# Optimization experiments

Measured on AMD Instinct MI355X. Metric: run time of the kernel, lower is better.

Reference implementation:

```python
import jax, jax.numpy as jnp
import numpy as np

P_MINUS_1 = 1.0      # p=2 -> (p-1)
LCP_BETA = 32.0
LOG_ALPHA = float(np.log(2.0))  # alpha=2.0
KDIG = 8
N_HEAD = 16


def _rope(x, cos, sin):
    # x: (B,T,H,D), cos/sin: (T,D//2)
    d = x.shape[-1] // 2
    x1, x2 = x[..., :d], x[..., d:]
    c = cos[None, :, None, :]
    s = sin[None, :, None, :]
    return jnp.concatenate([x1 * c - x2 * s, x1 * s + x2 * c], axis=-1)


def _rms_norm(x, eps=1e-6):
    return x * jax.lax.rsqrt(jnp.mean(jnp.square(x), axis=-1, keepdims=True) + eps)


def setup_inputs() -> dict:
    key = jax.random.key(0)
    ks = jax.random.split(key, 9)
    B, T, C, H = 2, 512, 1024, N_HEAD
    D = C // H
    std = 0.02
    x = jax.random.normal(ks[0], (B, T, C), jnp.float32)
    cos = jax.random.uniform(ks[1], (T, D // 2), jnp.float32)
    sin = jax.random.uniform(ks[2], (T, D // 2), jnp.float32)
    Wq = jax.random.normal(ks[3], (C, C), jnp.float32) * std
    Wk = jax.random.normal(ks[4], (C, C), jnp.float32) * std
    Wv = jax.random.normal(ks[5], (C, C), jnp.float32) * std
    Wo = jax.random.normal(ks[6], (C, C), jnp.float32) * std
    # to_digits_* use flax default lecun_normal: std = 1/sqrt(fan_in)
    Wdq = jax.random.normal(ks[7], (D, KDIG), jnp.float32) / np.sqrt(D)
    Wdk = jax.random.normal(ks[8], (D, KDIG), jnp.float32) / np.sqrt(D)
    return {"x": x, "cos": cos, "sin": sin, "Wq": Wq, "Wk": Wk, "Wv": Wv,
            "Wo": Wo, "Wdq": Wdq, "Wdk": Wdk}


def _soft_lcp_depth(q_digits, k_digits):
    # q_digits: (B,H,Tq,K), k_digits: (B,H,Tk,K) -> (B,H,Tq,Tk)
    diff = jnp.abs(q_digits[:, :, :, None, :] - k_digits[:, :, None, :, :])
    match_prob = jnp.exp(-LCP_BETA * jnp.square(diff))
    prefix_prob = jnp.cumprod(match_prob, axis=-1)
    return jnp.sum(prefix_prob, axis=-1)


def reference(x, cos, sin, Wq, Wk, Wv, Wo, Wdq, Wdk):
    B, T, C = x.shape
    H = N_HEAD
    D = C // H
    q = (x @ Wq).reshape(B, T, H, D)
    k = (x @ Wk).reshape(B, T, H, D)
    v = (x @ Wv).reshape(B, T, H, D)
    q = _rms_norm(_rope(q, cos, sin))
    k = _rms_norm(_rope(k, cos, sin))
    q = jnp.transpose(q, (0, 2, 1, 3))  # (B,H,T,D)
    k = jnp.transpose(k, (0, 2, 1, 3))
    v = jnp.transpose(v, (0, 2, 1, 3))
    # causal keep mask (T,T), broadcast over (B,H)
    keep = jnp.tril(jnp.ones((T, T), dtype=bool))[None, None]
    q_digits = jax.nn.sigmoid((q @ Wdq).astype(jnp.float32)) * P_MINUS_1
    k_digits = jax.nn.sigmoid((k @ Wdk).astype(jnp.float32)) * P_MINUS_1
    lcp = _soft_lcp_depth(q_digits, k_digits)  # (B,H,T,T)
    weights = jnp.exp(lcp * LOG_ALPHA)
    weights = jnp.where(keep, weights, 0.0)
    denom = jnp.maximum(jnp.sum(weights, axis=-1, keepdims=True), 1e-9)
    attn = weights / denom
    y = jnp.einsum('bhqk,bhkd->bhqd', attn.astype(v.dtype), v)
    y = jnp.transpose(y, (0, 2, 1, 3)).reshape(B, T, C)
    return y @ Wo
```

## Files before the change

### kernel.cpp

```cpp
#include <hip/hip_runtime.h>

#define T_SEQ 512
#define CDIM  1024
#define NH    16
#define DH    64
#define BB    2
#define KD    8

#define BETA_LOG2E 46.16624131f
#define LOG2E      1.4426950408889634f

typedef unsigned short u16;
typedef __attribute__((ext_vector_type(8))) short bf16x8;
typedef __attribute__((ext_vector_type(4))) float f32x4;

__device__ inline u16 f2bf(float f) {
    unsigned int u = __builtin_bit_cast(unsigned int, f);
    unsigned int r = (u + 0x7fffu + ((u >> 16) & 1u)) >> 16;
    return (u16)r;
}
__device__ inline float bf2f(u16 v) {
    unsigned int u = ((unsigned int)v) << 16;
    return __builtin_bit_cast(float, u);
}

__device__ inline void gload_lds16(const void* g, void* l) {
    __builtin_amdgcn_global_load_lds(
        (const __attribute__((address_space(1))) void*)g,
        (__attribute__((address_space(3))) void*)l, 16, 0, 0);
}

__global__ __launch_bounds__(256)
void prep_kernel(const float* __restrict__ x,
                 const float* __restrict__ W0, const float* __restrict__ W1,
                 const float* __restrict__ W2, const float* __restrict__ W3,
                 u16* __restrict__ xb,
                 u16* __restrict__ T0, u16* __restrict__ T1,
                 u16* __restrict__ T2, u16* __restrict__ T3)
{
    const int tid = threadIdx.x;
    if (blockIdx.z == 4) {
        const int row = blockIdx.y * 32 + (tid >> 3);
        const int col = blockIdx.x * 32 + (tid & 7) * 4;
        float4 v = *(const float4*)&x[(size_t)row * CDIM + col];
        ushort4 o = { f2bf(v.x), f2bf(v.y), f2bf(v.z), f2bf(v.w) };
        *(ushort4*)&xb[(size_t)row * CDIM + col] = o;
        return;
    }
    __shared__ u16 tile[32][33];
    const float* W = (blockIdx.z == 0) ? W0 : (blockIdx.z == 1) ? W1
                   : (blockIdx.z == 2) ? W2 : W3;
    u16* Tt        = (blockIdx.z == 0) ? T0 : (blockIdx.z == 1) ? T1
                   : (blockIdx.z == 2) ? T2 : T3;
    const int k0 = blockIdx.y * 32, n0 = blockIdx.x * 32;
    const int r = tid >> 3, c4 = (tid & 7) * 4;

    float4 v = *(const float4*)&W[(size_t)(k0 + r) * CDIM + n0 + c4];
    tile[r][c4 + 0] = f2bf(v.x);
    tile[r][c4 + 1] = f2bf(v.y);
    tile[r][c4 + 2] = f2bf(v.z);
    tile[r][c4 + 3] = f2bf(v.w);
    __syncthreads();
    ushort4 o;
    o.x = tile[c4 + 0][r];
    o.y = tile[c4 + 1][r];
    o.z = tile[c4 + 2][r];
    o.w = tile[c4 + 3][r];
    *(ushort4*)&Tt[(size_t)(n0 + r) * CDIM + k0 + c4] = o;
}

__global__ __launch_bounds__(256)
void gemm_qkv_fused(const u16* __restrict__ A,
                    const u16* __restrict__ Bq, const u16* __restrict__ Bk,
                    const u16* __restrict__ Bv,
                    const float* __restrict__ cosp, const float* __restrict__ sinp,
                    const float* __restrict__ Wdq, const float* __restrict__ Wdk,
                    float* __restrict__ qdig, float* __restrict__ kdig,
                    u16* __restrict__ Vt)
{
    __shared__ __align__(16) char smem[32768];
    u16* As = (u16*)smem;
    u16* Bs = As + 8192;
    float* Cf = (float*)smem;

    const int wg = (blockIdx.x & 7) * 96 + (blockIdx.x >> 3);
    const int z = wg >> 8;
    const int rem = wg & 255;
    const int h = rem & 15;
    const int m0 = (rem >> 4) * 64;
    const int n0 = h * 64;

    const u16* Bt = (z == 0) ? Bq : (z == 1) ? Bk : Bv;

    const int tid = threadIdx.x;
    const int l = tid & 63, w = tid >> 6;
    const int wr = (w >> 1) * 32, wc = (w & 1) * 32;

    f32x4 acc[2][2];
    #pragma unroll
    for (int i = 0; i < 2; ++i)
        #pragma unroll
        for (int j = 0; j < 2; ++j)
            acc[i][j] = (f32x4){0.f, 0.f, 0.f, 0.f};

    for (int k0 = 0; k0 < CDIM; k0 += 128) {
        __syncthreads();
        #pragma unroll
        for (int q = 0; q < 4; ++q) {
            const int row = w * 16 + q * 4 + (l >> 4);
            const int slot = (l & 15) ^ (row & 15);
            gload_lds16(A  + (size_t)(m0 + row) * CDIM + k0 + slot * 8,
                        &As[(w * 16 + q * 4) * 128]);
            gload_lds16(Bt + (size_t)(n0 + row) * CDIM + k0 + slot * 8,
                        &Bs[(w * 16 + q * 4) * 128]);
        }
        __syncthreads();

        #pragma unroll
        for (int kh = 0; kh < 4; ++kh) {
            bf16x8 af[2], bfr[2];
            #pragma unroll
            for (int i = 0; i < 2; ++i) {
                const int ra = wr + i * 16 + (l & 15);
                const int sa = (kh * 4 + (l >> 4)) ^ (ra & 15);
                af[i] = *(const bf16x8*)&As[ra * 128 + sa * 8];
                const int rb = wc + i * 16 + (l & 15);
                const int sb = (kh * 4 + (l >> 4)) ^ (rb & 15);
                bfr[i] = *(const bf16x8*)&Bs[rb * 128 + sb * 8];
            }
            #pragma unroll
            for (int i = 0; i < 2; ++i)
                #pragma unroll
                for (int j = 0; j < 2; ++j)
                    acc[i][j] = __builtin_amdgcn_mfma_f32_16x16x32_bf16(
                        af[i], bfr[j], acc[i][j], 0, 0, 0);
        }
    }

    __syncthreads();

    if (z == 2) {
        #pragma unroll
        for (int i = 0; i < 2; ++i)
            #pragma unroll
            for (int j = 0; j < 2; ++j) {
                const int mm = wr + i * 16 + (l >> 4) * 4;
                const int dd = wc + j * 16 + (l & 15);
                #pragma unroll
                for (int r = 0; r < 4; ++r)
                    Cf[dd * 65 + mm + r] = acc[i][j][r];
            }
        __syncthreads();
        const int b = m0 >> 9, t0 = m0 & (T_SEQ - 1);
        u16* vbase = Vt + ((size_t)(b * NH + h) * 64) * T_SEQ;
        #pragma unroll
        for (int it = 0; it < 16; ++it) {
            const int d = it * 4 + w;
            vbase[(size_t)d * T_SEQ + t0 + l] = f2bf(Cf[d * 65 + l]);
        }
        return;
    }

    #pragma unroll
    for (int i = 0; i < 2; ++i)
        #pragma unroll
        for (int j = 0; j < 2; ++j) {
            const int mm = wr + i * 16 + (l >> 4) * 4;
            const int dd = wc + j * 16 + (l & 15);
            #pragma unroll
            for (int r = 0; r < 4; ++r)
                Cf[(mm + r) * 65 + dd] = acc[i][j][r];
        }

    const float* Wd = z ? Wdk : Wdq;
    float* dig = z ? kdig : qdig;

    const int dl = l & 15, rq = l >> 4;
    float wreg[4][8];
    #pragma unroll
    for (int d4 = 0; d4 < 4; ++d4) {
        *(float4*)&wreg[d4][0] = *(const float4*)&Wd[(dl + d4 * 16) * 8];
        *(float4*)&wreg[d4][4] = *(const float4*)&Wd[(dl + d4 * 16) * 8 + 4];
    }
    __syncthreads();

    for (int g = 0; g < 4; ++g) {
        const int m = w * 16 + g * 4 + rq;
        const int mg = m0 + m;
        const int b = mg >> 9, t = mg & (T_SEQ - 1);

        const float* cr = &Cf[m * 65];
        float r0 = cr[dl], r1 = cr[dl + 16], r2 = cr[dl + 32], r3 = cr[dl + 48];
        float c0 = cosp[t * 32 + dl], c1 = cosp[t * 32 + dl + 16];
        float s0 = sinp[t * 32 + dl], s1 = sinp[t * 32 + dl + 16];
        float v0 = r0 * c0 - r2 * s0;
        float v1 = r1 * c1 - r3 * s1;
        float v2 = r0 * s0 + r2 * c0;
        float v3 = r1 * s1 + r3 * c1;

        float ss = v0 * v0 + v1 * v1 + v2 * v2 + v3 * v3;
        #pragma unroll
        for (int off = 1; off < 16; off <<= 1) ss += __shfl_xor(ss, off);
        float sc = rsqrtf(ss * (1.0f / 64.0f) + 1e-6f);
        v0 *= sc; v1 *= sc; v2 *= sc; v3 *= sc;

        float zz[8];
        #pragma unroll
        for (int j = 0; j < 8; ++j)
            zz[j] = v0 * wreg[0][j] + v1 * wreg[1][j] + v2 * wreg[2][j] + v3 * wreg[3][j];
        #pragma unroll
        for (int j = 0; j < 8; ++j) {
            #pragma unroll
            for (int off = 1; off < 16; off <<= 1) zz[j] += __shfl_xor(zz[j], off);
        }
        float zsel = zz[0];
        #pragma unroll
        for (int j = 1; j < 8; ++j) zsel = (dl == j) ? zz[j] : zsel;
        if (dl < 8)
            dig[((size_t)(b * NH + h) * T_SEQ + t) * KD + dl] =
                1.0f / (1.0f + exp2f(-LOG2E * zsel));
    }
}

__global__ __launch_bounds__(256)
void attn_partial(const float* __restrict__ qdig, const float* __restrict__ kdig,
                  const u16* __restrict__ Vt,
                  u16* __restrict__ pacc, float* __restrict__ pdeng)
{
    __shared__ u16 Vs[4096];
    __shared__ u16 Ps[4096];
    __shared__ float qds[512];

    const int tid = threadIdx.x;
    const int w = tid >> 6, l = tid & 63;

    const int wg = (blockIdx.x & 7) * 144 + (blockIdx.x >> 3);
    const int tile = wg % 36;
    const int bh = wg / 36;
    const size_t bhT = (size_t)bh * T_SEQ;

    int id = tile, c = 0;
    while (id >= c + 1) { id -= (c + 1); ++c; }
    const int kt = id;
    const int k0 = kt * 64;

    const int srow = l >> 3, sslot = (l & 7) ^ srow;
    #pragma unroll
    for (int q2 = 0; q2 < 2; ++q2) {
        const int R0 = w * 16 + q2 * 8;
        gload_lds16(Vt + ((size_t)bh * 64 + R0 + srow) * T_SEQ + k0 + sslot * 8,
                    &Vs[R0 * 64]);
    }
    *(float2*)&qds[tid * 2] = *(const float2*)&qdig[(bhT + c * 64) * KD + tid * 2];

    float kd[8];
    {
        const float* kp = &kdig[(bhT + k0 + l) * KD];
        *(float4*)&kd[0] = *(const float4*)kp;
        *(float4*)&kd[4] = *(const float4*)(kp + 4);
    }
    __syncthreads();

    const bool diag = (kt == c);
    for (int qi = 0; qi < 16; ++qi) {
        const int qrow = w * 16 + qi;
        float qd[8];
        *(float4*)&qd[0] = *(const float4*)&qds[qrow * 8];
        *(float4*)&qd[4] = *(const float4*)&qds[qrow * 8 + 4];
        float S = 0.f, lcp = 0.f;
        #pragma unroll
        for (int jj = 0; jj < 8; ++jj) {
            float d = qd[jj] - kd[jj];
            S += d * d;
            lcp += exp2f(-BETA_LOG2E * S);
        }
        float wgt = exp2f(lcp);
        if (diag && l > qrow) wgt = 0.f;
        Ps[qrow * 64 + (((l >> 3) ^ (qi & 7)) << 3) + (l & 7)] = f2bf(wgt);
    }
    __syncthreads();

    const int wr = (w >> 1) * 32, wc = (w & 1) * 32;
    f32x4 acc[2][2], accd[2];
    #pragma unroll
    for (int i = 0; i < 2; ++i) {
        accd[i] = (f32x4){0.f, 0.f, 0.f, 0.f};
        #pragma unroll
        for (int j = 0; j < 2; ++j) acc[i][j] = (f32x4){0.f, 0.f, 0.f, 0.f};
    }
    bf16x8 ones;
    #pragma unroll
    for (int i = 0; i < 8; ++i) ones[i] = (short)0x3F80;

    #pragma unroll
    for (int kh = 0; kh < 2; ++kh) {
        bf16x8 af[2], bfr[2];
        #pragma unroll
        for (int i = 0; i < 2; ++i) {
            const int ra = wr + i * 16 + (l & 15);
            const int sa = (kh * 4 + (l >> 4)) ^ (ra & 7);
            af[i] = *(const bf16x8*)&Ps[ra * 64 + sa * 8];
            const int rb = wc + i * 16 + (l & 15);
            const int sb = (kh * 4 + (l >> 4)) ^ (rb & 7);
            bfr[i] = *(const bf16x8*)&Vs[rb * 64 + sb * 8];
        }
        #pragma unroll
        for (int i = 0; i < 2; ++i) {
            accd[i] = __builtin_amdgcn_mfma_f32_16x16x32_bf16(af[i], ones, accd[i], 0, 0, 0);
            #pragma unroll
            for (int j = 0; j < 2; ++j)
                acc[i][j] = __builtin_amdgcn_mfma_f32_16x16x32_bf16(
                    af[i], bfr[j], acc[i][j], 0, 0, 0);
        }
    }

    const int task = bh * 36 + tile;
    u16* pa = pacc + (size_t)task * 4096;
    #pragma unroll
    for (int i = 0; i < 2; ++i) {
        const int row = wr + i * 16 + (l >> 4) * 4;
        #pragma unroll
        for (int j = 0; j < 2; ++j) {
            const int col = wc + j * 16 + (l & 15);
            #pragma unroll
            for (int r = 0; r < 4; ++r)
                pa[(size_t)(row + r) * 64 + col] = f2bf(acc[i][j][r]);
        }
        if ((l & 15) == 0) {
            #pragma unroll
            for (int r = 0; r < 4; ++r)
                pdeng[(size_t)task * 64 + row + r] = accd[i][r];
        }
    }
}

__global__ __launch_bounds__(256)
void attn_combine(const u16* __restrict__ pacc, const float* __restrict__ pdeng,
                  u16* __restrict__ y)
{
    const int c = blockIdx.x >> 1, half = blockIdx.x & 1;
    const int h = blockIdx.y, b = blockIdx.z;
    const int tid = threadIdx.x;
    const int r = tid >> 2, cg = (tid & 3) * 8 + half * 32;
    const int base = (b * NH + h) * 36 + c * (c + 1) / 2;

    float acc[8] = {};
    float den = 0.f;
    for (int kt = 0; kt <= c; ++kt) {
        const u16* pa = pacc + (size_t)(base + kt) * 4096 + r * 64 + cg;
        ushort4 v0 = *(const ushort4*)(pa + 0);
        ushort4 v1 = *(const ushort4*)(pa + 4);
        acc[0] += bf2f(v0.x); acc[1] += bf2f(v0.y);
        acc[2] += bf2f(v0.z); acc[3] += bf2f(v0.w);
        acc[4] += bf2f(v1.x); acc[5] += bf2f(v1.y);
        acc[6] += bf2f(v1.z); acc[7] += bf2f(v1.w);
        den += pdeng[(size_t)(base + kt) * 64 + r];
    }
    float inv = 1.f / fmaxf(den, 1e-9f);

    u16* yr = y + ((size_t)(b * T_SEQ + c * 64 + r)) * CDIM + h * DH + cg;
    uint4 p;
    p.x = f2bf(acc[0] * inv) | ((unsigned)f2bf(acc[1] * inv) << 16);
    p.y = f2bf(acc[2] * inv) | ((unsigned)f2bf(acc[3] * inv) << 16);
    p.z = f2bf(acc[4] * inv) | ((unsigned)f2bf(acc[5] * inv) << 16);
    p.w = f2bf(acc[6] * inv) | ((unsigned)f2bf(acc[7] * inv) << 16);
    *(uint4*)yr = p;
}

__global__ __launch_bounds__(256)
void gemm_proj(const u16* __restrict__ A, const u16* __restrict__ Bt,
               float* __restrict__ C)
{
    __shared__ u16 As[32 * 128];
    __shared__ u16 Bs[64 * 128];

    const int wg = (blockIdx.x & 7) * 64 + (blockIdx.x >> 3);
    const int n0 = (wg & 15) * 64;
    const int m0 = (wg >> 4) * 32;

    const int tid = threadIdx.x;
    const int l = tid & 63, w = tid >> 6;
    const int wr = (w & 1) * 16, wc = (w >> 1) * 32;

    f32x4 acc[2];
    acc[0] = (f32x4){0.f, 0.f, 0.f, 0.f};
    acc[1] = (f32x4){0.f, 0.f, 0.f, 0.f};

    for (int k0 = 0; k0 < CDIM; k0 += 128) {
        __syncthreads();
        #pragma unroll
        for (int q = 0; q < 2; ++q) {
            const int rowa = w * 8 + q * 4 + (l >> 4);
            const int slota = (l & 15) ^ (rowa & 15);
            gload_lds16(A + (size_t)(m0 + rowa) * CDIM + k0 + slota * 8,
                        &As[(w * 8 + q * 4) * 128]);
        }
        #pragma unroll
        for (int q = 0; q < 4; ++q) {
            const int row = w * 16 + q * 4 + (l >> 4);
            const int slot = (l & 15) ^ (row & 15);
            gload_lds16(Bt + (size_t)(n0 + row) * CDIM + k0 + slot * 8,
                        &Bs[(w * 16 + q * 4) * 128]);
        }
        __syncthreads();

        #pragma unroll
        for (int kh = 0; kh < 4; ++kh) {
            const int ra = wr + (l & 15);
            const int sa = (kh * 4 + (l >> 4)) ^ (ra & 15);
            bf16x8 af = *(const bf16x8*)&As[ra * 128 + sa * 8];
            #pragma unroll
            for (int j = 0; j < 2; ++j) {
                const int rb = wc + j * 16 + (l & 15);
                const int sb = (kh * 4 + (l >> 4)) ^ (rb & 15);
                bf16x8 bfr = *(const bf16x8*)&Bs[rb * 128 + sb * 8];
                acc[j] = __builtin_amdgcn_mfma_f32_16x16x32_bf16(
                    af, bfr, acc[j], 0, 0, 0);
            }
        }
    }

    #pragma unroll
    for (int j = 0; j < 2; ++j) {
        const int row = m0 + wr + (l >> 4) * 4;
        const int col = n0 + wc + j * 16 + (l & 15);
        #pragma unroll
        for (int r = 0; r < 4; ++r)
            C[(size_t)(row + r) * CDIM + col] = acc[j][r];
    }
}

extern "C" void kernel_launch(void* const* d_in, const int* in_sizes, int n_in,
                              void* d_out, int out_size, void* d_ws, size_t ws_size,
                              hipStream_t stream)
{
    (void)in_sizes; (void)n_in; (void)out_size; (void)ws_size;
    const float* x    = (const float*)d_in[0];
    const float* cosp = (const float*)d_in[1];
    const float* sinp = (const float*)d_in[2];
    const float* Wq   = (const float*)d_in[3];
    const float* Wk   = (const float*)d_in[4];
    const float* Wv   = (const float*)d_in[5];
    const float* Wo   = (const float*)d_in[6];
    const float* Wdq  = (const float*)d_in[7];
    const float* Wdk  = (const float*)d_in[8];
    float* out = (float*)d_out;

    const int M = BB * T_SEQ;
    const size_t MC = (size_t)M * CDIM;
    char* p = (char*)d_ws;
    float* qdig = (float*)p; p += (size_t)M * NH * KD * 4;
    float* kdig = (float*)p; p += (size_t)M * NH * KD * 4;
    u16* xb   = (u16*)p; p += MC * 2;
    u16* wqt  = (u16*)p; p += MC * 2;
    u16* wkt  = (u16*)p; p += MC * 2;
    u16* wvt  = (u16*)p; p += MC * 2;
    u16* wot  = (u16*)p; p += MC * 2;
    u16* Vt   = (u16*)p; p += MC * 2;
    u16* ybuf = (u16*)p; p += MC * 2;
    u16* pacc = (u16*)p; p += (size_t)1152 * 4096 * 2;
    float* pdeng = (float*)p; p += (size_t)1152 * 64 * 4;

    dim3 blk(256);
    prep_kernel<<<dim3(32, 32, 5), blk, 0, stream>>>(
        x, Wq, Wk, Wv, Wo, xb, wqt, wkt, wvt, wot);
    gemm_qkv_fused<<<dim3(768), blk, 0, stream>>>(
        xb, wqt, wkt, wvt, cosp, sinp, Wdq, Wdk, qdig, kdig, Vt);
    attn_partial<<<dim3(1152), blk, 0, stream>>>(
        qdig, kdig, Vt, pacc, pdeng);
    attn_combine<<<dim3(16, NH, BB), blk, 0, stream>>>(pacc, pdeng, ybuf);
    gemm_proj<<<dim3(512), blk, 0, stream>>>(ybuf, wot, out);
}
```

Baseline: 58.72 us.

## Double-buffer GEMM K-loops and fuse attention combine via last-block atomic counter

Both the QKV and projection GEMMs now use a double-buffered K-loop with 64-wide K tiles. Each loop prefetches the next tile with global-to-LDS loads while the current one is consumed, and uses partial vmcnt waits instead of two full syncthreads per iteration. The separate attn_combine kernel is removed. The last attn_partial block to finish for each query tile, detected through an atomic counter zeroed in prep_kernel, performs the reduction and normalization. This removes one kernel launch and overlaps load latency with MFMA work, at the cost of atomics, threadfences and a serialized tail reduction in the winning block.

New measurement: 120.2 us. +104.8%, slower.

```diff
diff --git a/kernel.cpp b/kernel.cpp
--- a/kernel.cpp
+++ b/kernel.cpp
@@ -36,10 +36,12 @@
                  const float* __restrict__ W2, const float* __restrict__ W3,
                  u16* __restrict__ xb,
                  u16* __restrict__ T0, u16* __restrict__ T1,
-                 u16* __restrict__ T2, u16* __restrict__ T3)
+                 u16* __restrict__ T2, u16* __restrict__ T3,
+                 int* __restrict__ cnt)
 {
     const int tid = threadIdx.x;
     if (blockIdx.z == 4) {
+        if (blockIdx.x == 0 && blockIdx.y == 0) cnt[tid] = 0;
         const int row = blockIdx.y * 32 + (tid >> 3);
         const int col = blockIdx.x * 32 + (tid & 7) * 4;
         float4 v = *(const float4*)&x[(size_t)row * CDIM + col];
@@ -95,6 +97,8 @@
     const int tid = threadIdx.x;
     const int l = tid & 63, w = tid >> 6;
     const int wr = (w >> 1) * 32, wc = (w & 1) * 32;
+    const int srow = l >> 3;
+    const int sslot = (l & 7) ^ srow;
 
     f32x4 acc[2][2];
     #pragma unroll
@@ -103,40 +107,53 @@
         for (int j = 0; j < 2; ++j)
             acc[i][j] = (f32x4){0.f, 0.f, 0.f, 0.f};
 
-    for (int k0 = 0; k0 < CDIM; k0 += 128) {
-        __syncthreads();
-        #pragma unroll
-        for (int q = 0; q < 4; ++q) {
-            const int row = w * 16 + q * 4 + (l >> 4);
-            const int slot = (l & 15) ^ (row & 15);
-            gload_lds16(A  + (size_t)(m0 + row) * CDIM + k0 + slot * 8,
-                        &As[(w * 16 + q * 4) * 128]);
-            gload_lds16(Bt + (size_t)(n0 + row) * CDIM + k0 + slot * 8,
-                        &Bs[(w * 16 + q * 4) * 128]);
-        }
-        __syncthreads();
-
-        #pragma unroll
-        for (int kh = 0; kh < 4; ++kh) {
-            bf16x8 af[2], bfr[2];
-            #pragma unroll
-            for (int i = 0; i < 2; ++i) {
+    auto STAGE = [&](int buf, int k0) {
+        #pragma unroll
+        for (int q = 0; q < 2; ++q) {
+            const int row = w * 16 + q * 8 + srow;
+            gload_lds16(A  + (size_t)(m0 + row) * CDIM + k0 + sslot * 8,
+                        &As[buf * 4096 + (w * 16 + q * 8) * 64]);
+            gload_lds16(Bt + (size_t)(n0 + row) * CDIM + k0 + sslot * 8,
+                        &Bs[buf * 4096 + (w * 16 + q * 8) * 64]);
+        }
+    };
+
+    STAGE(0, 0);
+    for (int t = 0; t < 16; ++t) {
+        const int cur = t & 1;
+        if (t < 15) {
+            STAGE(cur ^ 1, (t + 1) * 64);
+            asm volatile("s_waitcnt vmcnt(4)" ::: "memory");
+        } else {
+            asm volatile("s_waitcnt vmcnt(0)" ::: "memory");
+        }
+        __builtin_amdgcn_sched_barrier(0);
+        __builtin_amdgcn_s_barrier();
+
+        const u16* Ab = &As[cur * 4096];
+        const u16* Bb = &Bs[cur * 4096];
+        bf16x8 af[2][2], bfr[2][2];
+        #pragma unroll
+        for (int i = 0; i < 2; ++i)
+            #pragma unroll
+            for (int kh = 0; kh < 2; ++kh) {
                 const int ra = wr + i * 16 + (l & 15);
-                const int sa = (kh * 4 + (l >> 4)) ^ (ra & 15);
-                af[i] = *(const bf16x8*)&As[ra * 128 + sa * 8];
+                const int sa = (kh * 4 + (l >> 4)) ^ (ra & 7);
+                af[i][kh] = *(const bf16x8*)&Ab[ra * 64 + sa * 8];
                 const int rb = wc + i * 16 + (l & 15);
-                const int sb = (kh * 4 + (l >> 4)) ^ (rb & 15);
-                bfr[i] = *(const bf16x8*)&Bs[rb * 128 + sb * 8];
+                const int sb = (kh * 4 + (l >> 4)) ^ (rb & 7);
+                bfr[i][kh] = *(const bf16x8*)&Bb[rb * 64 + sb * 8];
             }
+        #pragma unroll
+        for (int kh = 0; kh < 2; ++kh)
             #pragma unroll
             for (int i = 0; i < 2; ++i)
                 #pragma unroll
                 for (int j = 0; j < 2; ++j)
                     acc[i][j] = __builtin_amdgcn_mfma_f32_16x16x32_bf16(
-                        af[i], bfr[j], acc[i][j], 0, 0, 0);
-        }
-    }
-
+                        af[i][kh], bfr[j][kh], acc[i][j], 0, 0, 0);
+        __builtin_amdgcn_s_barrier();
+    }
     __syncthreads();
 
     if (z == 2) {
@@ -225,11 +242,13 @@
 __global__ __launch_bounds__(256)
 void attn_partial(const float* __restrict__ qdig, const float* __restrict__ kdig,
                   const u16* __restrict__ Vt,
-                  u16* __restrict__ pacc, float* __restrict__ pdeng)
+                  u16* __restrict__ pacc, float* __restrict__ pdeng,
+                  int* __restrict__ cnt, u16* __restrict__ y)
 {
     __shared__ u16 Vs[4096];
     __shared__ u16 Ps[4096];
     __shared__ float qds[512];
+    __shared__ int winflag;
 
     const int tid = threadIdx.x;
     const int w = tid >> 6, l = tid & 63;
@@ -332,47 +351,59 @@
                 pdeng[(size_t)task * 64 + row + r] = accd[i][r];
         }
     }
-}
-
-__global__ __launch_bounds__(256)
-void attn_combine(const u16* __restrict__ pacc, const float* __restrict__ pdeng,
-                  u16* __restrict__ y)
-{
-    const int c = blockIdx.x >> 1, half = blockIdx.x & 1;
-    const int h = blockIdx.y, b = blockIdx.z;
-    const int tid = threadIdx.x;
-    const int r = tid >> 2, cg = (tid & 3) * 8 + half * 32;
-    const int base = (b * NH + h) * 36 + c * (c + 1) / 2;
-
-    float acc[8] = {};
+
+    __syncthreads();
+    if (tid == 0) {
+        __threadfence();
+        int old = atomicAdd(&cnt[bh * 8 + c], 1);
+        winflag = (old == c) ? 1 : 0;
+    }
+    __syncthreads();
+    if (!winflag) return;
+    __threadfence();
+
+    const int r = tid >> 2, cg = (tid & 3) * 16;
+    const int base = bh * 36 + c * (c + 1) / 2;
+    float accf[16] = {};
     float den = 0.f;
-    for (int kt = 0; kt <= c; ++kt) {
-        const u16* pa = pacc + (size_t)(base + kt) * 4096 + r * 64 + cg;
-        ushort4 v0 = *(const ushort4*)(pa + 0);
-        ushort4 v1 = *(const ushort4*)(pa + 4);
-        acc[0] += bf2f(v0.x); acc[1] += bf2f(v0.y);
-        acc[2] += bf2f(v0.z); acc[3] += bf2f(v0.w);
-        acc[4] += bf2f(v1.x); acc[5] += bf2f(v1.y);
-        acc[6] += bf2f(v1.z); acc[7] += bf2f(v1.w);
-        den += pdeng[(size_t)(base + kt) * 64 + r];
+    for (int k2 = 0; k2 <= c; ++k2) {
+        const u16* ps = pacc + (size_t)(base + k2) * 4096 + r * 64 + cg;
+        ushort4 v0 = *(const ushort4*)(ps + 0);
+        ushort4 v1 = *(const ushort4*)(ps + 4);
+        ushort4 v2 = *(const ushort4*)(ps + 8);
+        ushort4 v3 = *(const ushort4*)(ps + 12);
+        accf[0]  += bf2f(v0.x); accf[1]  += bf2f(v0.y);
+        accf[2]  += bf2f(v0.z); accf[3]  += bf2f(v0.w);
+        accf[4]  += bf2f(v1.x); accf[5]  += bf2f(v1.y);
+        accf[6]  += bf2f(v1.z); accf[7]  += bf2f(v1.w);
+        accf[8]  += bf2f(v2.x); accf[9]  += bf2f(v2.y);
+        accf[10] += bf2f(v2.z); accf[11] += bf2f(v2.w);
+        accf[12] += bf2f(v3.x); accf[13] += bf2f(v3.y);
+        accf[14] += bf2f(v3.z); accf[15] += bf2f(v3.w);
+        den += pdeng[(size_t)(base + k2) * 64 + r];
     }
     float inv = 1.f / fmaxf(den, 1e-9f);
 
+    const int b = bh >> 4, h = bh & 15;
     u16* yr = y + ((size_t)(b * T_SEQ + c * 64 + r)) * CDIM + h * DH + cg;
-    uint4 p;
-    p.x = f2bf(acc[0] * inv) | ((unsigned)f2bf(acc[1] * inv) << 16);
-    p.y = f2bf(acc[2] * inv) | ((unsigned)f2bf(acc[3] * inv) << 16);
-    p.z = f2bf(acc[4] * inv) | ((unsigned)f2bf(acc[5] * inv) << 16);
-    p.w = f2bf(acc[6] * inv) | ((unsigned)f2bf(acc[7] * inv) << 16);
-    *(uint4*)yr = p;
+    uint4 p0, p1;
+    p0.x = f2bf(accf[0] * inv)  | ((unsigned)f2bf(accf[1] * inv)  << 16);
+    p0.y = f2bf(accf[2] * inv)  | ((unsigned)f2bf(accf[3] * inv)  << 16);
+    p0.z = f2bf(accf[4] * inv)  | ((unsigned)f2bf(accf[5] * inv)  << 16);
+    p0.w = f2bf(accf[6] * inv)  | ((unsigned)f2bf(accf[7] * inv)  << 16);
+    p1.x = f2bf(accf[8] * inv)  | ((unsigned)f2bf(accf[9] * inv)  << 16);
+    p1.y = f2bf(accf[10] * inv) | ((unsigned)f2bf(accf[11] * inv) << 16);
+    p1.z = f2bf(accf[12] * inv) | ((unsigned)f2bf(accf[13] * inv) << 16);
+    p1.w = f2bf(accf[14] * inv) | ((unsigned)f2bf(accf[15] * inv) << 16);
+    *(uint4*)(yr + 0) = p0;
+    *(uint4*)(yr + 8) = p1;
 }
 
 __global__ __launch_bounds__(256)
 void gemm_proj(const u16* __restrict__ A, const u16* __restrict__ Bt,
                float* __restrict__ C)
 {
-    __shared__ u16 As[32 * 128];
-    __shared__ u16 Bs[64 * 128];
+    __shared__ __align__(16) u16 S[12288];
 
     const int wg = (blockIdx.x & 7) * 64 + (blockIdx.x >> 3);
     const int n0 = (wg & 15) * 64;
@@ -381,43 +412,54 @@
     const int tid = threadIdx.x;
     const int l = tid & 63, w = tid >> 6;
     const int wr = (w & 1) * 16, wc = (w >> 1) * 32;
+    const int srow = l >> 3;
+    const int sslot = (l & 7) ^ srow;
 
     f32x4 acc[2];
     acc[0] = (f32x4){0.f, 0.f, 0.f, 0.f};
     acc[1] = (f32x4){0.f, 0.f, 0.f, 0.f};
 
-    for (int k0 = 0; k0 < CDIM; k0 += 128) {
-        __syncthreads();
+    auto STAGE = [&](int buf, int k0) {
+        const int rowa = w * 8 + srow;
+        gload_lds16(A + (size_t)(m0 + rowa) * CDIM + k0 + sslot * 8,
+                    &S[buf * 2048 + (w * 8) * 64]);
         #pragma unroll
         for (int q = 0; q < 2; ++q) {
-            const int rowa = w * 8 + q * 4 + (l >> 4);
-            const int slota = (l & 15) ^ (rowa & 15);
-            gload_lds16(A + (size_t)(m0 + rowa) * CDIM + k0 + slota * 8,
-                        &As[(w * 8 + q * 4) * 128]);
-        }
-        #pragma unroll
-        for (int q = 0; q < 4; ++q) {
-            const int row = w * 16 + q * 4 + (l >> 4);
-            const int slot = (l & 15) ^ (row & 15);
-            gload_lds16(Bt + (size_t)(n0 + row) * CDIM + k0 + slot * 8,
-                        &Bs[(w * 16 + q * 4) * 128]);
-        }
-        __syncthreads();
-
-        #pragma unroll
-        for (int kh = 0; kh < 4; ++kh) {
+            const int row = w * 16 + q * 8 + srow;
+            gload_lds16(Bt + (size_t)(n0 + row) * CDIM + k0 + sslot * 8,
+                        &S[4096 + buf * 4096 + (w * 16 + q * 8) * 64]);
+        }
+    };
+
+    STAGE(0, 0);
+    for (int t = 0; t < 16; ++t) {
+        const int cur = t & 1;
+        if (t < 15) {
+            STAGE(cur ^ 1, (t + 1) * 64);
+            asm volatile("s_waitcnt vmcnt(3)" ::: "memory");
+        } else {
+            asm volatile("s_waitcnt vmcnt(0)" ::: "memory");
+        }
+        __builtin_amdgcn_sched_barrier(0);
+        __builtin_amdgcn_s_barrier();
+
+        const u16* Ab = &S[cur * 2048];
+        const u16* Bb = &S[4096 + cur * 4096];
+        #pragma unroll
+        for (int kh = 0; kh < 2; ++kh) {
             const int ra = wr + (l & 15);
-            const int sa = (kh * 4 + (l >> 4)) ^ (ra & 15);
-            bf16x8 af = *(const bf16x8*)&As[ra * 128 + sa * 8];
+            const int sa = (kh * 4 + (l >> 4)) ^ (ra & 7);
+            bf16x8 af = *(const bf16x8*)&Ab[ra * 64 + sa * 8];
             #pragma unroll
             for (int j = 0; j < 2; ++j) {
                 const int rb = wc + j * 16 + (l & 15);
-                const int sb = (kh * 4 + (l >> 4)) ^ (rb & 15);
-                bf16x8 bfr = *(const bf16x8*)&Bs[rb * 128 + sb * 8];
+                const int sb = (kh * 4 + (l >> 4)) ^ (rb & 7);
+                bf16x8 bfr = *(const bf16x8*)&Bb[rb * 64 + sb * 8];
                 acc[j] = __builtin_amdgcn_mfma_f32_16x16x32_bf16(
                     af, bfr, acc[j], 0, 0, 0);
             }
         }
+        __builtin_amdgcn_s_barrier();
     }
 
     #pragma unroll
@@ -460,14 +502,14 @@
     u16* ybuf = (u16*)p; p += MC * 2;
     u16* pacc = (u16*)p; p += (size_t)1152 * 4096 * 2;
     float* pdeng = (float*)p; p += (size_t)1152 * 64 * 4;
+    int* cnt = (int*)p; p += 256 * 4;
 
     dim3 blk(256);
     prep_kernel<<<dim3(32, 32, 5), blk, 0, stream>>>(
-        x, Wq, Wk, Wv, Wo, xb, wqt, wkt, wvt, wot);
+        x, Wq, Wk, Wv, Wo, xb, wqt, wkt, wvt, wot, cnt);
     gemm_qkv_fused<<<dim3(768), blk, 0, stream>>>(
         xb, wqt, wkt, wvt, cosp, sinp, Wdq, Wdk, qdig, kdig, Vt);
     attn_partial<<<dim3(1152), blk, 0, stream>>>(
-        qdig, kdig, Vt, pacc, pdeng);
-    attn_combine<<<dim3(16, NH, BB), blk, 0, stream>>>(pacc, pdeng, ybuf);
+        qdig, kdig, Vt, pacc, pdeng, cnt, ybuf);
     gemm_proj<<<dim3(512), blk, 0, stream>>>(ybuf, wot, out);
 }
```
